# Kernel optimization log

Measured on AMD Instinct MI355X. Metric: run time of the kernel, lower is better.

## Reference

```python
import jax, jax.numpy as jnp
import numpy as np

B, D_IN, D_OUT, E, K, H = 8192, 1024, 1024, 8, 2, 2048


def setup_inputs() -> dict:
    key = jax.random.key(0)
    ks = jax.random.split(key, 7)
    s_in = 1.0 / np.sqrt(D_IN)
    s_h = 1.0 / np.sqrt(H)
    return {
        "x": jax.random.normal(ks[0], (B, D_IN), dtype=jnp.float32),
        "Wg": jax.random.uniform(ks[1], (D_IN, E), minval=-s_in, maxval=s_in, dtype=jnp.float32),
        "bg": jax.random.uniform(ks[2], (E,), minval=-s_in, maxval=s_in, dtype=jnp.float32),
        "W1": jax.random.uniform(ks[3], (E, D_IN, H), minval=-s_in, maxval=s_in, dtype=jnp.float32),
        "b1": jax.random.uniform(ks[4], (E, H), minval=-s_in, maxval=s_in, dtype=jnp.float32),
        "W2": jax.random.uniform(ks[5], (E, H, D_OUT), minval=-s_h, maxval=s_h, dtype=jnp.float32),
        "b2": jax.random.uniform(ks[6], (E, D_OUT), minval=-s_h, maxval=s_h, dtype=jnp.float32),
    }


def reference(x, Wg, bg, W1, b1, W2, b2):
    # gating: linear then top-k -> binary mask (scores are NOT used as weights)
    gate_scores = x @ Wg + bg                      # [B, E]
    _, topk_idx = jax.lax.top_k(gate_scores, K)    # [B, K]
    mask = jax.nn.one_hot(topk_idx, E, dtype=x.dtype).sum(axis=-2)  # [B, E]

    # dense compute of ALL experts (faithful to original module)
    h = jax.nn.relu(jnp.einsum('bi,eih->beh', x, W1) + b1[None])    # [B, E, H]
    expert_out = jnp.einsum('beh,eho->beo', h, W2) + b2[None]       # [B, E, D_OUT]

    # mask to top-k experts and sum over experts
    return jnp.einsum('beo,be->bo', expert_out, mask)               # [B, D_OUT]
```

## Files before the change

### kernel.cpp

```cpp
#include <hip/hip_runtime.h>


#define NTOK 8192
#define DIN  1024
#define DOUT 1024
#define NEXP 8
#define NHID 2048
#define NENT (NTOK * 2)
#define ABLK 64
#define MCHMAX 136

typedef __bf16 bf16_t;
typedef __bf16 bf16x8 __attribute__((ext_vector_type(8)));
typedef __bf16 bf16x4 __attribute__((ext_vector_type(4)));
typedef float  f32x4  __attribute__((ext_vector_type(4)));

#define AS3(p) ((__attribute__((address_space(3))) void*)(unsigned)(unsigned long long)(p))
#define AS1(p) ((__attribute__((address_space(1))) void*)(unsigned long long)(p))

static __device__ __forceinline__ int imin_(int a, int b) { return a < b ? a : b; }

static __device__ __forceinline__ int xcd_swizzle() {
    int cpx = gridDim.x >> 3;
    return (blockIdx.x & 7) * cpx + (blockIdx.x >> 3);
}

__global__ __launch_bounds__(256) void k_transpose_cvt(
    const float* __restrict__ W, bf16_t* __restrict__ WT, int K_, int N_)
{
    __shared__ float tile[64][65];
    const int tilesK = K_ >> 6, tilesN = N_ >> 6;
    int bid = blockIdx.x;
    int e = bid / (tilesK * tilesN);
    int r = bid % (tilesK * tilesN);
    int tk = (r / tilesN) << 6;
    int tn = (r % tilesN) << 6;
    const float* Wb  = W  + (size_t)e * K_ * N_;
    bf16_t*      WTb = WT + (size_t)e * K_ * N_;
    int lr = threadIdx.x >> 6;
    int lc = threadIdx.x & 63;
#pragma unroll
    for (int i = 0; i < 16; ++i) {
        int row = i * 4 + lr;
        tile[row][lc] = Wb[(size_t)(tk + row) * N_ + tn + lc];
    }
    __syncthreads();
#pragma unroll
    for (int i = 0; i < 16; ++i) {
        int row = i * 4 + lr;
        WTb[(size_t)(tn + row) * K_ + tk + lc] = (bf16_t)tile[lc][row];
    }
}

__global__ __launch_bounds__(256) void k_wgT(
    const float* __restrict__ Wg, float* __restrict__ WgT)
{
    int i = blockIdx.x * 256 + threadIdx.x;
    int d = i >> 3, e = i & 7;
    WgT[e * DIN + d] = Wg[i];
}

__global__ __launch_bounds__(256) void k_gating(
    const float* __restrict__ x, const float* __restrict__ WgT,
    const float* __restrict__ bg, bf16_t* __restrict__ xb,
    int* __restrict__ topk)
{
    int lane = threadIdx.x & 63;
    int tok  = blockIdx.x * 4 + (threadIdx.x >> 6);
    const float* xr  = x  + (size_t)tok * DIN;
    bf16_t*      xbr = xb + (size_t)tok * DIN;

    float4 xv[4];
#pragma unroll
    for (int i = 0; i < 4; ++i) {
        int idx = i * 256 + lane * 4;
        xv[i] = *reinterpret_cast<const float4*>(xr + idx);
        bf16x4 o;
        o[0] = (bf16_t)xv[i].x; o[1] = (bf16_t)xv[i].y;
        o[2] = (bf16_t)xv[i].z; o[3] = (bf16_t)xv[i].w;
        *reinterpret_cast<bf16x4*>(xbr + idx) = o;
    }

    float acc[NEXP];
#pragma unroll
    for (int e = 0; e < NEXP; ++e) {
        const float* we = WgT + (size_t)e * DIN;
        float a = 0.f;
#pragma unroll
        for (int i = 0; i < 4; ++i) {
            int idx = i * 256 + lane * 4;
            float4 w = *reinterpret_cast<const float4*>(we + idx);
            a += xv[i].x * w.x + xv[i].y * w.y + xv[i].z * w.z + xv[i].w * w.w;
        }
        acc[e] = a;
    }

#pragma unroll
    for (int e = 0; e < NEXP; ++e) {
#pragma unroll
        for (int off = 32; off >= 1; off >>= 1) acc[e] += __shfl_xor(acc[e], off);
    }
    if (lane == 0) {
        float s[NEXP];
#pragma unroll
        for (int e = 0; e < NEXP; ++e) s[e] = acc[e] + bg[e];
        int e0 = 0;
        for (int e = 1; e < NEXP; ++e) if (s[e] > s[e0]) e0 = e;
        int e1 = (e0 == 0) ? 1 : 0;
        for (int e = 0; e < NEXP; ++e) if (e != e0 && s[e] > s[e1]) e1 = e;
        topk[2 * tok]     = e0;
        topk[2 * tok + 1] = e1;
    }
}

__global__ __launch_bounds__(256) void k_hist(
    const int* __restrict__ topk, int* __restrict__ bh)
{
    __shared__ int h[NEXP];
    if (threadIdx.x < NEXP) h[threadIdx.x] = 0;
    __syncthreads();
    int i = blockIdx.x * 256 + threadIdx.x;
    atomicAdd(&h[topk[i]], 1);
    __syncthreads();
    if (threadIdx.x < NEXP) bh[blockIdx.x * NEXP + threadIdx.x] = h[threadIdx.x];
}

__global__ void k_scan2(const int* __restrict__ bh, int* __restrict__ counts,
                        int* __restrict__ offsets, int* __restrict__ blockbase,
                        int* __restrict__ chtab, int* __restrict__ nch)
{
    __shared__ int sc[NEXP], so_[NEXP + 1];
    int t = threadIdx.x;
    if (t < NEXP) {
        int s = 0;
        for (int b = 0; b < ABLK; ++b) s += bh[b * NEXP + t];
        sc[t] = s;
    }
    __syncthreads();
    if (t == 0) {
        int s = 0;
        for (int e = 0; e < NEXP; ++e) { so_[e] = s; s += sc[e]; }
        so_[NEXP] = s;
        for (int e = 0; e <= NEXP; ++e) offsets[e] = so_[e];
        for (int e = 0; e < NEXP; ++e) counts[e] = sc[e];
    }
    __syncthreads();
    if (t < NEXP) {
        int run = so_[t];
        for (int b = 0; b < ABLK; ++b) {
            blockbase[b * NEXP + t] = run;
            run += bh[b * NEXP + t];
        }
    }
    __syncthreads();
    if (t == 0) {
        int n = 0;
        for (int e = 0; e < NEXP; ++e) {
            int mch = (sc[e] + 127) >> 7;
            for (int m = 0; m < mch; ++m) chtab[n++] = (e << 16) | m;
        }
        nch[0] = n;
    }
}

__global__ __launch_bounds__(256) void k_assign(
    const int* __restrict__ topk, const int* __restrict__ blockbase,
    int* __restrict__ token_ids, int* __restrict__ slot_of)
{
    __shared__ int wcnt[4][NEXP];
    int tid = threadIdx.x, blk = blockIdx.x;
    int i = blk * 256 + tid;
    int e = topk[i];
    int lane = tid & 63, w = tid >> 6;
    unsigned long long ltmask = (1ull << lane) - 1ull;
    int rank_w = 0;
#pragma unroll
    for (int ee = 0; ee < NEXP; ++ee) {
        unsigned long long m = __ballot(e == ee);
        if (ee == e) rank_w = (int)__popcll(m & ltmask);
        if (lane == 0) wcnt[w][ee] = (int)__popcll(m);
    }
    __syncthreads();
    int pre = 0;
    for (int wv = 0; wv < w; ++wv) pre += wcnt[wv][e];
    int s = blockbase[blk * NEXP + e] + pre + rank_w;
    token_ids[s] = i >> 1;
    slot_of[i] = s;
}

__global__ __launch_bounds__(256, 4) void k_gemm1(
    const bf16_t* __restrict__ xb, const bf16_t* __restrict__ w1t,
    const float* __restrict__ b1, bf16_t* __restrict__ hb,
    const int* __restrict__ token_ids, const int* __restrict__ counts,
    const int* __restrict__ offsets, const int* __restrict__ chtab,
    const int* __restrict__ nch)
{
    int bid   = xcd_swizzle();
    int chunk = bid >> 4;
    int nc    = bid & 15;
    if (chunk >= nch[0]) return;
    int em = chtab[chunk];
    int e  = em >> 16;
    int mc = em & 0xffff;
    int count = counts[e];
    int base  = offsets[e];

    __shared__ short At[128][32];
    __shared__ short Bt[128][32];

    int t    = threadIdx.x;
    int lane = t & 63;
    int w    = t >> 6;
    int wr   = (w >> 1) * 64;
    int wc   = (w & 1) * 64;

    int r0 = t >> 2;
    int r1 = 64 + r0;
    int c0 = (t & 3) * 8;

    int row0 = imin_(mc * 128 + r0, count - 1);
    int row1 = imin_(mc * 128 + r1, count - 1);
    const bf16_t* a0 = xb + (size_t)token_ids[base + row0] * DIN + c0;
    const bf16_t* a1 = xb + (size_t)token_ids[base + row1] * DIN + c0;
    const bf16_t* wbase = w1t + (size_t)e * NHID * DIN;
    const bf16_t* bp0 = wbase + (size_t)(nc * 128 + r0) * DIN + c0;
    const bf16_t* bp1 = wbase + (size_t)(nc * 128 + r1) * DIN + c0;

    unsigned lds0 = (unsigned)(t & 192) * 16;
    unsigned lds1 = 4096u + lds0;

    f32x4 acc[4][4];
#pragma unroll
    for (int m = 0; m < 4; ++m)
#pragma unroll
        for (int n = 0; n < 4; ++n) acc[m][n] = (f32x4){0.f, 0.f, 0.f, 0.f};

    char* AtB = (char*)&At[0][0];
    char* BtB = (char*)&Bt[0][0];

    for (int k0 = 0; k0 < DIN; k0 += 32) {
        __builtin_amdgcn_global_load_lds(AS1(a0 + k0),  AS3(AtB + lds0), 16, 0, 0);
        __builtin_amdgcn_global_load_lds(AS1(a1 + k0),  AS3(AtB + lds1), 16, 0, 0);
        __builtin_amdgcn_global_load_lds(AS1(bp0 + k0), AS3(BtB + lds0), 16, 0, 0);
        __builtin_amdgcn_global_load_lds(AS1(bp1 + k0), AS3(BtB + lds1), 16, 0, 0);
        __syncthreads();

        bf16x8 af[4], bfv[4];
        int kr = (lane >> 4) * 8;
#pragma unroll
        for (int m = 0; m < 4; ++m)
            af[m] = *reinterpret_cast<const bf16x8*>(&At[wr + m * 16 + (lane & 15)][kr]);
#pragma unroll
        for (int n = 0; n < 4; ++n)
            bfv[n] = *reinterpret_cast<const bf16x8*>(&Bt[wc + n * 16 + (lane & 15)][kr]);
#pragma unroll
        for (int m = 0; m < 4; ++m)
#pragma unroll
            for (int n = 0; n < 4; ++n)
                acc[m][n] = __builtin_amdgcn_mfma_f32_16x16x32_bf16(af[m], bfv[n], acc[m][n], 0, 0, 0);
        __syncthreads();
    }

    int cl = lane & 15;
    int rq = (lane >> 4) * 4;
#pragma unroll
    for (int n = 0; n < 4; ++n) {
        int col  = nc * 128 + wc + n * 16 + cl;
        float bias = b1[e * NHID + col];
#pragma unroll
        for (int m = 0; m < 4; ++m) {
            int rbase = mc * 128 + wr + m * 16 + rq;
#pragma unroll
            for (int q = 0; q < 4; ++q) {
                int gr = rbase + q;
                if (gr < count) {
                    float v = acc[m][n][q] + bias;
                    v = v > 0.f ? v : 0.f;
                    hb[(size_t)(base + gr) * NHID + col] = (bf16_t)v;
                }
            }
        }
    }
}

__global__ __launch_bounds__(256, 4) void k_gemm2(
    const bf16_t* __restrict__ hb, const bf16_t* __restrict__ w2t,
    bf16_t* __restrict__ so,
    const int* __restrict__ counts, const int* __restrict__ offsets,
    const int* __restrict__ chtab, const int* __restrict__ nch)
{
    int bid   = xcd_swizzle();
    int chunk = bid >> 3;
    int nc    = bid & 7;
    if (chunk >= nch[0]) return;
    int em = chtab[chunk];
    int e  = em >> 16;
    int mc = em & 0xffff;
    int count = counts[e];
    int base  = offsets[e];

    __shared__ short At[128][32];
    __shared__ short Bt[128][32];

    int t    = threadIdx.x;
    int lane = t & 63;
    int w    = t >> 6;
    int wr   = (w >> 1) * 64;
    int wc   = (w & 1) * 64;

    int r0 = t >> 2;
    int r1 = 64 + r0;
    int c0 = (t & 3) * 8;

    int row0 = imin_(mc * 128 + r0, count - 1);
    int row1 = imin_(mc * 128 + r1, count - 1);
    const bf16_t* a0 = hb + (size_t)(base + row0) * NHID + c0;
    const bf16_t* a1 = hb + (size_t)(base + row1) * NHID + c0;
    const bf16_t* wbase = w2t + (size_t)e * DOUT * NHID;
    const bf16_t* bp0 = wbase + (size_t)(nc * 128 + r0) * NHID + c0;
    const bf16_t* bp1 = wbase + (size_t)(nc * 128 + r1) * NHID + c0;

    unsigned lds0 = (unsigned)(t & 192) * 16;
    unsigned lds1 = 4096u + lds0;

    f32x4 acc[4][4];
#pragma unroll
    for (int m = 0; m < 4; ++m)
#pragma unroll
        for (int n = 0; n < 4; ++n) acc[m][n] = (f32x4){0.f, 0.f, 0.f, 0.f};

    char* AtB = (char*)&At[0][0];
    char* BtB = (char*)&Bt[0][0];

    for (int k0 = 0; k0 < NHID; k0 += 32) {
        __builtin_amdgcn_global_load_lds(AS1(a0 + k0),  AS3(AtB + lds0), 16, 0, 0);
        __builtin_amdgcn_global_load_lds(AS1(a1 + k0),  AS3(AtB + lds1), 16, 0, 0);
        __builtin_amdgcn_global_load_lds(AS1(bp0 + k0), AS3(BtB + lds0), 16, 0, 0);
        __builtin_amdgcn_global_load_lds(AS1(bp1 + k0), AS3(BtB + lds1), 16, 0, 0);
        __syncthreads();

        bf16x8 af[4], bfv[4];
        int kr = (lane >> 4) * 8;
#pragma unroll
        for (int m = 0; m < 4; ++m)
            af[m] = *reinterpret_cast<const bf16x8*>(&At[wr + m * 16 + (lane & 15)][kr]);
#pragma unroll
        for (int n = 0; n < 4; ++n)
            bfv[n] = *reinterpret_cast<const bf16x8*>(&Bt[wc + n * 16 + (lane & 15)][kr]);
#pragma unroll
        for (int m = 0; m < 4; ++m)
#pragma unroll
            for (int n = 0; n < 4; ++n)
                acc[m][n] = __builtin_amdgcn_mfma_f32_16x16x32_bf16(af[m], bfv[n], acc[m][n], 0, 0, 0);
        __syncthreads();
    }

    int cl = lane & 15;
    int rq = (lane >> 4) * 4;
#pragma unroll
    for (int n = 0; n < 4; ++n) {
        int col = nc * 128 + wc + n * 16 + cl;
#pragma unroll
        for (int m = 0; m < 4; ++m) {
            int rbase = mc * 128 + wr + m * 16 + rq;
#pragma unroll
            for (int q = 0; q < 4; ++q) {
                int gr = rbase + q;
                if (gr < count)
                    so[(size_t)(base + gr) * DOUT + col] = (bf16_t)acc[m][n][q];
            }
        }
    }
}

__global__ __launch_bounds__(256) void k_combine(
    const bf16_t* __restrict__ so, const float* __restrict__ b2,
    const int* __restrict__ topk, const int* __restrict__ slot_of,
    float* __restrict__ out)
{
    int tid = threadIdx.x;
    int tok = blockIdx.x * 2 + (tid >> 7);
    int c0  = (tid & 127) * 8;
    int s0 = slot_of[2 * tok],  s1 = slot_of[2 * tok + 1];
    int e0 = topk[2 * tok],     e1 = topk[2 * tok + 1];
    bf16x8 a = *reinterpret_cast<const bf16x8*>(so + (size_t)s0 * DOUT + c0);
    bf16x8 b = *reinterpret_cast<const bf16x8*>(so + (size_t)s1 * DOUT + c0);
    const float* bb0 = b2 + (size_t)e0 * DOUT + c0;
    const float* bb1 = b2 + (size_t)e1 * DOUT + c0;
    float* op = out + (size_t)tok * DOUT + c0;
    float4 o0, o1;
    o0.x = (float)a[0] + (float)b[0] + bb0[0] + bb1[0];
    o0.y = (float)a[1] + (float)b[1] + bb0[1] + bb1[1];
    o0.z = (float)a[2] + (float)b[2] + bb0[2] + bb1[2];
    o0.w = (float)a[3] + (float)b[3] + bb0[3] + bb1[3];
    o1.x = (float)a[4] + (float)b[4] + bb0[4] + bb1[4];
    o1.y = (float)a[5] + (float)b[5] + bb0[5] + bb1[5];
    o1.z = (float)a[6] + (float)b[6] + bb0[6] + bb1[6];
    o1.w = (float)a[7] + (float)b[7] + bb0[7] + bb1[7];
    *reinterpret_cast<float4*>(op)     = o0;
    *reinterpret_cast<float4*>(op + 4) = o1;
}

extern "C" void kernel_launch(void* const* d_in, const int* in_sizes, int n_in,
                              void* d_out, int out_size, void* d_ws, size_t ws_size,
                              hipStream_t stream)
{
    const float* x  = (const float*)d_in[0];
    const float* Wg = (const float*)d_in[1];
    const float* bg = (const float*)d_in[2];
    const float* W1 = (const float*)d_in[3];
    const float* b1 = (const float*)d_in[4];
    const float* W2 = (const float*)d_in[5];
    const float* b2 = (const float*)d_in[6];
    float* out = (float*)d_out;

    char* ws = (char*)d_ws;
    bf16_t* xb        = (bf16_t*)(ws);
    bf16_t* w1t       = (bf16_t*)(ws + 16777216);
    bf16_t* w2t       = (bf16_t*)(ws + 50331648);
    bf16_t* hb        = (bf16_t*)(ws + 83886080);
    int*    topk      = (int*)(ws + 150994944);
    int*    counts    = (int*)(ws + 151060480);
    int*    offsets   = (int*)(ws + 151060544);
    int*    token_ids = (int*)(ws + 151060608);
    int*    bh        = (int*)(ws + 151126144);
    int*    blockbase = (int*)(ws + 151128192);
    int*    slot_of   = (int*)(ws + 151130240);

    int* chtab = bh;
    int* nch   = bh + MCHMAX;

    bf16_t* so = (bf16_t*)ws;
    float* wgT = (float*)hb;

    k_wgT<<<(DIN * NEXP) / 256, 256, 0, stream>>>(Wg, wgT);

    k_transpose_cvt<<<NEXP * (DIN / 64) * (NHID / 64), 256, 0, stream>>>(W1, w1t, DIN, NHID);
    k_transpose_cvt<<<NEXP * (NHID / 64) * (DOUT / 64), 256, 0, stream>>>(W2, w2t, NHID, DOUT);

    k_gating<<<NTOK / 4, 256, 0, stream>>>(x, wgT, bg, xb, topk);
    k_hist<<<ABLK, 256, 0, stream>>>(topk, bh);
    k_scan2<<<1, 64, 0, stream>>>(bh, counts, offsets, blockbase, chtab, nch);
    k_assign<<<ABLK, 256, 0, stream>>>(topk, blockbase, token_ids, slot_of);

    k_gemm1<<<MCHMAX * 16, 256, 0, stream>>>(
        xb, w1t, b1, hb, token_ids, counts, offsets, chtab, nch);
    k_gemm2<<<MCHMAX * 8, 256, 0, stream>>>(
        hb, w2t, so, counts, offsets, chtab, nch);
    k_combine<<<NTOK / 2, 256, 0, stream>>>(so, b2, topk, slot_of, out);
}
```

Measured before the change: 312.0 us.

## Triple-buffer LDS tiles in both expert GEMMs with async prefetch pipeline

Both grouped GEMM kernels move from a single LDS tile with load-then-sync-per-iteration to a three-stage ring buffer. Tiles are prefetched two K-steps ahead through global_load_lds, with explicit vmcnt waits and raw s_barrier in place of __syncthreads. The goal is to overlap global memory latency with MFMA work. In exchange LDS use triples to 48KB per block and the launch-bounds occupancy hint drops from 4 to 3 blocks. The hand-written waitcnt and barrier sequence relies on the compiler not reordering or adding vm loads.

Measured after the change: 294.3 us. -5.7%, faster.

```diff
diff --git a/kernel.cpp b/kernel.cpp
--- a/kernel.cpp
+++ b/kernel.cpp
@@ -188,7 +188,7 @@
     slot_of[i] = s;
 }
 
-__global__ __launch_bounds__(256, 4) void k_gemm1(
+__global__ __launch_bounds__(256, 3) void k_gemm1(
     const bf16_t* __restrict__ xb, const bf16_t* __restrict__ w1t,
     const float* __restrict__ b1, bf16_t* __restrict__ hb,
     const int* __restrict__ token_ids, const int* __restrict__ counts,
@@ -205,8 +205,8 @@
     int count = counts[e];
     int base  = offsets[e];
 
-    __shared__ short At[128][32];
-    __shared__ short Bt[128][32];
+    __shared__ short At[3][128][32];
+    __shared__ short Bt[3][128][32];
 
     int t    = threadIdx.x;
     int lane = t & 63;
@@ -235,31 +235,53 @@
 #pragma unroll
         for (int n = 0; n < 4; ++n) acc[m][n] = (f32x4){0.f, 0.f, 0.f, 0.f};
 
-    char* AtB = (char*)&At[0][0];
-    char* BtB = (char*)&Bt[0][0];
-
-    for (int k0 = 0; k0 < DIN; k0 += 32) {
-        __builtin_amdgcn_global_load_lds(AS1(a0 + k0),  AS3(AtB + lds0), 16, 0, 0);
-        __builtin_amdgcn_global_load_lds(AS1(a1 + k0),  AS3(AtB + lds1), 16, 0, 0);
-        __builtin_amdgcn_global_load_lds(AS1(bp0 + k0), AS3(BtB + lds0), 16, 0, 0);
-        __builtin_amdgcn_global_load_lds(AS1(bp1 + k0), AS3(BtB + lds1), 16, 0, 0);
-        __syncthreads();
+    char* AtB = (char*)&At[0][0][0];
+    char* BtB = (char*)&Bt[0][0][0];
+
+#define STAGE1(buf, koff) do {                                                                     \
+    unsigned bo_ = (unsigned)(buf) * 8192u;                                                        \
+    __builtin_amdgcn_global_load_lds(AS1(a0  + (koff)), AS3(AtB + bo_ + lds0), 16, 0, 0);          \
+    __builtin_amdgcn_global_load_lds(AS1(a1  + (koff)), AS3(AtB + bo_ + lds1), 16, 0, 0);          \
+    __builtin_amdgcn_global_load_lds(AS1(bp0 + (koff)), AS3(BtB + bo_ + lds0), 16, 0, 0);          \
+    __builtin_amdgcn_global_load_lds(AS1(bp1 + (koff)), AS3(BtB + bo_ + lds1), 16, 0, 0);          \
+  } while (0)
+
+    constexpr int NK = DIN / 32;
+    STAGE1(0, 0);
+    STAGE1(1, 32);
+    int cc = 0;
+    int cs = 2;
+
+    for (int kt = 0; kt < NK; ++kt) {
+        if (kt + 2 < NK) {
+            STAGE1(cs, (kt + 2) * 32);
+            asm volatile("s_waitcnt vmcnt(8)" ::: "memory");
+        } else if (kt + 2 == NK) {
+            asm volatile("s_waitcnt vmcnt(4)" ::: "memory");
+        } else {
+            asm volatile("s_waitcnt vmcnt(0)" ::: "memory");
+        }
+        __builtin_amdgcn_s_barrier();
 
         bf16x8 af[4], bfv[4];
         int kr = (lane >> 4) * 8;
 #pragma unroll
         for (int m = 0; m < 4; ++m)
-            af[m] = *reinterpret_cast<const bf16x8*>(&At[wr + m * 16 + (lane & 15)][kr]);
+            af[m] = *reinterpret_cast<const bf16x8*>(&At[cc][wr + m * 16 + (lane & 15)][kr]);
 #pragma unroll
         for (int n = 0; n < 4; ++n)
-            bfv[n] = *reinterpret_cast<const bf16x8*>(&Bt[wc + n * 16 + (lane & 15)][kr]);
+            bfv[n] = *reinterpret_cast<const bf16x8*>(&Bt[cc][wc + n * 16 + (lane & 15)][kr]);
 #pragma unroll
         for (int m = 0; m < 4; ++m)
 #pragma unroll
             for (int n = 0; n < 4; ++n)
                 acc[m][n] = __builtin_amdgcn_mfma_f32_16x16x32_bf16(af[m], bfv[n], acc[m][n], 0, 0, 0);
-        __syncthreads();
-    }
+
+        __builtin_amdgcn_s_barrier();
+        cs = cc;
+        cc = (cc == 2) ? 0 : cc + 1;
+    }
+#undef STAGE1
 
     int cl = lane & 15;
     int rq = (lane >> 4) * 4;
@@ -283,7 +305,7 @@
     }
 }
 
-__global__ __launch_bounds__(256, 4) void k_gemm2(
+__global__ __launch_bounds__(256, 3) void k_gemm2(
     const bf16_t* __restrict__ hb, const bf16_t* __restrict__ w2t,
     bf16_t* __restrict__ so,
     const int* __restrict__ counts, const int* __restrict__ offsets,
@@ -299,8 +321,8 @@
     int count = counts[e];
     int base  = offsets[e];
 
-    __shared__ short At[128][32];
-    __shared__ short Bt[128][32];
+    __shared__ short At[3][128][32];
+    __shared__ short Bt[3][128][32];
 
     int t    = threadIdx.x;
     int lane = t & 63;
@@ -329,31 +351,53 @@
 #pragma unroll
         for (int n = 0; n < 4; ++n) acc[m][n] = (f32x4){0.f, 0.f, 0.f, 0.f};
 
-    char* AtB = (char*)&At[0][0];
-    char* BtB = (char*)&Bt[0][0];
-
-    for (int k0 = 0; k0 < NHID; k0 += 32) {
-        __builtin_amdgcn_global_load_lds(AS1(a0 + k0),  AS3(AtB + lds0), 16, 0, 0);
-        __builtin_amdgcn_global_load_lds(AS1(a1 + k0),  AS3(AtB + lds1), 16, 0, 0);
-        __builtin_amdgcn_global_load_lds(AS1(bp0 + k0), AS3(BtB + lds0), 16, 0, 0);
-        __builtin_amdgcn_global_load_lds(AS1(bp1 + k0), AS3(BtB + lds1), 16, 0, 0);
-        __syncthreads();
+    char* AtB = (char*)&At[0][0][0];
+    char* BtB = (char*)&Bt[0][0][0];
+
+#define STAGE2(buf, koff) do {                                                                     \
+    unsigned bo_ = (unsigned)(buf) * 8192u;                                                        \
+    __builtin_amdgcn_global_load_lds(AS1(a0  + (koff)), AS3(AtB + bo_ + lds0), 16, 0, 0);          \
+    __builtin_amdgcn_global_load_lds(AS1(a1  + (koff)), AS3(AtB + bo_ + lds1), 16, 0, 0);          \
+    __builtin_amdgcn_global_load_lds(AS1(bp0 + (koff)), AS3(BtB + bo_ + lds0), 16, 0, 0);          \
+    __builtin_amdgcn_global_load_lds(AS1(bp1 + (koff)), AS3(BtB + bo_ + lds1), 16, 0, 0);          \
+  } while (0)
+
+    constexpr int NK = NHID / 32;
+    STAGE2(0, 0);
+    STAGE2(1, 32);
+    int cc = 0;
+    int cs = 2;
+
+    for (int kt = 0; kt < NK; ++kt) {
+        if (kt + 2 < NK) {
+            STAGE2(cs, (kt + 2) * 32);
+            asm volatile("s_waitcnt vmcnt(8)" ::: "memory");
+        } else if (kt + 2 == NK) {
+            asm volatile("s_waitcnt vmcnt(4)" ::: "memory");
+        } else {
+            asm volatile("s_waitcnt vmcnt(0)" ::: "memory");
+        }
+        __builtin_amdgcn_s_barrier();
 
         bf16x8 af[4], bfv[4];
         int kr = (lane >> 4) * 8;
 #pragma unroll
         for (int m = 0; m < 4; ++m)
-            af[m] = *reinterpret_cast<const bf16x8*>(&At[wr + m * 16 + (lane & 15)][kr]);
+            af[m] = *reinterpret_cast<const bf16x8*>(&At[cc][wr + m * 16 + (lane & 15)][kr]);
 #pragma unroll
         for (int n = 0; n < 4; ++n)
-            bfv[n] = *reinterpret_cast<const bf16x8*>(&Bt[wc + n * 16 + (lane & 15)][kr]);
+            bfv[n] = *reinterpret_cast<const bf16x8*>(&Bt[cc][wc + n * 16 + (lane & 15)][kr]);
 #pragma unroll
         for (int m = 0; m < 4; ++m)
 #pragma unroll
             for (int n = 0; n < 4; ++n)
                 acc[m][n] = __builtin_amdgcn_mfma_f32_16x16x32_bf16(af[m], bfv[n], acc[m][n], 0, 0, 0);
-        __syncthreads();
-    }
+
+        __builtin_amdgcn_s_barrier();
+        cs = cc;
+        cc = (cc == 2) ? 0 : cc + 1;
+    }
+#undef STAGE2
 
     int cl = lane & 15;
     int rq = (lane >> 4) * 4;
```

## Rewrite grouped expert GEMMs with 256x256 tiles, double-buffered LDS and swizzle

Applied to the files above, without the earlier changes.

Both expert GEMMs move from 128x128 tiles with K=32 single-buffered steps to 256x256 tiles with 512 threads, K=64 steps, and double-buffered LDS loaded via global_load_lds. Shared-memory layout uses an XOR swizzle to avoid bank conflicts, and the MFMA phases are interleaved with s_setprio and explicit barriers so the next tile loads while the current one computes. This cuts global/LDS traffic per FLOP and per-iteration sync overhead. The cost is 128KB of LDS per block and fewer blocks, which lowers occupancy and adds padding waste on the last chunk of each expert.

After: 337.2 us. +8.1%, slower.

```diff
diff --git a/kernel.cpp b/kernel.cpp
--- a/kernel.cpp
+++ b/kernel.cpp
@@ -8,7 +8,7 @@
 #define NHID 2048
 #define NENT (NTOK * 2)
 #define ABLK 64
-#define MCHMAX 136
+#define MCHMAX 72
 
 typedef __bf16 bf16_t;
 typedef __bf16 bf16x8 __attribute__((ext_vector_type(8)));
@@ -156,7 +156,7 @@
     if (t == 0) {
         int n = 0;
         for (int e = 0; e < NEXP; ++e) {
-            int mch = (sc[e] + 127) >> 7;
+            int mch = (sc[e] + 255) >> 8;
             for (int m = 0; m < mch; ++m) chtab[n++] = (e << 16) | m;
         }
         nch[0] = n;
@@ -188,106 +188,64 @@
     slot_of[i] = s;
 }
 
-__global__ __launch_bounds__(256, 4) void k_gemm1(
+
+#define GEMM_PHASES(NKV)                                                           \
+    for (int kt = 0; kt < NKV; ++kt) {                                             \
+        const short* Ac = &As[kt & 1][0][0];                                       \
+        const short* Bc = &Bs[kt & 1][0][0];                                       \
+        unsigned dstb = (unsigned)(((kt & 1) ^ 1) * 32768) + wb;                   \
+        bf16x8 b_[4][2];                                                           \
+        _Pragma("unroll")                                                          \
+        for (int ph = 0; ph < 4; ++ph) {                                           \
+            if (ph == 0) {                                                         \
+                if (kt + 1 < NKV) {                                                \
+                    int ko = (kt + 1) * 64;                                        \
+                    __builtin_amdgcn_global_load_lds(AS1(aP0 + ko), AS3(AB + dstb),         16, 0, 0); \
+                    __builtin_amdgcn_global_load_lds(AS1(aP1 + ko), AS3(AB + dstb + 8192),  16, 0, 0); \
+                    __builtin_amdgcn_global_load_lds(AS1(aP2 + ko), AS3(AB + dstb + 16384), 16, 0, 0); \
+                    __builtin_amdgcn_global_load_lds(AS1(aP3 + ko), AS3(AB + dstb + 24576), 16, 0, 0); \
+                    __builtin_amdgcn_global_load_lds(AS1(bP0 + ko), AS3(BB + dstb),         16, 0, 0); \
+                    __builtin_amdgcn_global_load_lds(AS1(bP1 + ko), AS3(BB + dstb + 8192),  16, 0, 0); \
+                    __builtin_amdgcn_global_load_lds(AS1(bP2 + ko), AS3(BB + dstb + 16384), 16, 0, 0); \
+                    __builtin_amdgcn_global_load_lds(AS1(bP3 + ko), AS3(BB + dstb + 24576), 16, 0, 0); \
+                }                                                                  \
+                _Pragma("unroll")                                                  \
+                for (int nf = 0; nf < 4; ++nf) {                                   \
+                    b_[nf][0] = *reinterpret_cast<const bf16x8*>(Bc + nf * 1024 + boff0);        \
+                    b_[nf][1] = *reinterpret_cast<const bf16x8*>(Bc + nf * 1024 + (boff0 ^ 32)); \
+                }                                                                  \
+            }                                                                      \
+            bf16x8 a_[2][2];                                                       \
+            _Pragma("unroll")                                                      \
+            for (int j = 0; j < 2; ++j) {                                          \
+                const short* ar = Ac + (ph * 2 + j) * 1024;                        \
+                a_[j][0] = *reinterpret_cast<const bf16x8*>(ar + aoff0);           \
+                a_[j][1] = *reinterpret_cast<const bf16x8*>(ar + (aoff0 ^ 32));    \
+            }                                                                      \
+            __builtin_amdgcn_s_barrier();                                          \
+            __builtin_amdgcn_s_setprio(1);                                         \
+            _Pragma("unroll")                                                      \
+            for (int j = 0; j < 2; ++j) {                                          \
+                _Pragma("unroll")                                                  \
+                for (int nf = 0; nf < 4; ++nf) {                                   \
+                    acc[ph * 2 + j][nf] = __builtin_amdgcn_mfma_f32_16x16x32_bf16( \
+                        a_[j][0], b_[nf][0], acc[ph * 2 + j][nf], 0, 0, 0);        \
+                    acc[ph * 2 + j][nf] = __builtin_amdgcn_mfma_f32_16x16x32_bf16( \
+                        a_[j][1], b_[nf][1], acc[ph * 2 + j][nf], 0, 0, 0);        \
+                }                                                                  \
+            }                                                                      \
+            __builtin_amdgcn_s_setprio(0);                                         \
+            if (ph == 3) asm volatile("s_waitcnt vmcnt(0)" ::: "memory");          \
+            __builtin_amdgcn_s_barrier();                                          \
+        }                                                                          \
+    }
+
+__global__ __launch_bounds__(512) void k_gemm1(
     const bf16_t* __restrict__ xb, const bf16_t* __restrict__ w1t,
     const float* __restrict__ b1, bf16_t* __restrict__ hb,
     const int* __restrict__ token_ids, const int* __restrict__ counts,
     const int* __restrict__ offsets, const int* __restrict__ chtab,
     const int* __restrict__ nch)
-{
-    int bid   = xcd_swizzle();
-    int chunk = bid >> 4;
-    int nc    = bid & 15;
-    if (chunk >= nch[0]) return;
-    int em = chtab[chunk];
-    int e  = em >> 16;
-    int mc = em & 0xffff;
-    int count = counts[e];
-    int base  = offsets[e];
-
-    __shared__ short At[128][32];
-    __shared__ short Bt[128][32];
-
-    int t    = threadIdx.x;
-    int lane = t & 63;
-    int w    = t >> 6;
-    int wr   = (w >> 1) * 64;
-    int wc   = (w & 1) * 64;
-
-    int r0 = t >> 2;
-    int r1 = 64 + r0;
-    int c0 = (t & 3) * 8;
-
-    int row0 = imin_(mc * 128 + r0, count - 1);
-    int row1 = imin_(mc * 128 + r1, count - 1);
-    const bf16_t* a0 = xb + (size_t)token_ids[base + row0] * DIN + c0;
-    const bf16_t* a1 = xb + (size_t)token_ids[base + row1] * DIN + c0;
-    const bf16_t* wbase = w1t + (size_t)e * NHID * DIN;
-    const bf16_t* bp0 = wbase + (size_t)(nc * 128 + r0) * DIN + c0;
-    const bf16_t* bp1 = wbase + (size_t)(nc * 128 + r1) * DIN + c0;
-
-    unsigned lds0 = (unsigned)(t & 192) * 16;
-    unsigned lds1 = 4096u + lds0;
-
-    f32x4 acc[4][4];
-#pragma unroll
-    for (int m = 0; m < 4; ++m)
-#pragma unroll
-        for (int n = 0; n < 4; ++n) acc[m][n] = (f32x4){0.f, 0.f, 0.f, 0.f};
-
-    char* AtB = (char*)&At[0][0];
-    char* BtB = (char*)&Bt[0][0];
-
-    for (int k0 = 0; k0 < DIN; k0 += 32) {
-        __builtin_amdgcn_global_load_lds(AS1(a0 + k0),  AS3(AtB + lds0), 16, 0, 0);
-        __builtin_amdgcn_global_load_lds(AS1(a1 + k0),  AS3(AtB + lds1), 16, 0, 0);
-        __builtin_amdgcn_global_load_lds(AS1(bp0 + k0), AS3(BtB + lds0), 16, 0, 0);
-        __builtin_amdgcn_global_load_lds(AS1(bp1 + k0), AS3(BtB + lds1), 16, 0, 0);
-        __syncthreads();
-
-        bf16x8 af[4], bfv[4];
-        int kr = (lane >> 4) * 8;
-#pragma unroll
-        for (int m = 0; m < 4; ++m)
-            af[m] = *reinterpret_cast<const bf16x8*>(&At[wr + m * 16 + (lane & 15)][kr]);
-#pragma unroll
-        for (int n = 0; n < 4; ++n)
-            bfv[n] = *reinterpret_cast<const bf16x8*>(&Bt[wc + n * 16 + (lane & 15)][kr]);
-#pragma unroll
-        for (int m = 0; m < 4; ++m)
-#pragma unroll
-            for (int n = 0; n < 4; ++n)
-                acc[m][n] = __builtin_amdgcn_mfma_f32_16x16x32_bf16(af[m], bfv[n], acc[m][n], 0, 0, 0);
-        __syncthreads();
-    }
-
-    int cl = lane & 15;
-    int rq = (lane >> 4) * 4;
-#pragma unroll
-    for (int n = 0; n < 4; ++n) {
-        int col  = nc * 128 + wc + n * 16 + cl;
-        float bias = b1[e * NHID + col];
-#pragma unroll
-        for (int m = 0; m < 4; ++m) {
-            int rbase = mc * 128 + wr + m * 16 + rq;
-#pragma unroll
-            for (int q = 0; q < 4; ++q) {
-                int gr = rbase + q;
-                if (gr < count) {
-                    float v = acc[m][n][q] + bias;
-                    v = v > 0.f ? v : 0.f;
-                    hb[(size_t)(base + gr) * NHID + col] = (bf16_t)v;
-                }
-            }
-        }
-    }
-}
-
-__global__ __launch_bounds__(256, 4) void k_gemm2(
-    const bf16_t* __restrict__ hb, const bf16_t* __restrict__ w2t,
-    bf16_t* __restrict__ so,
-    const int* __restrict__ counts, const int* __restrict__ offsets,
-    const int* __restrict__ chtab, const int* __restrict__ nch)
 {
     int bid   = xcd_swizzle();
     int chunk = bid >> 3;
@@ -299,75 +257,167 @@
     int count = counts[e];
     int base  = offsets[e];
 
-    __shared__ short At[128][32];
-    __shared__ short Bt[128][32];
+    __shared__ short As[2][256][64];
+    __shared__ short Bs[2][256][64];
 
     int t    = threadIdx.x;
+    int w    = t >> 6;
     int lane = t & 63;
+    int wrM  = (w >> 2) * 128;
+    int wcN  = (w & 3) * 64;
+    int lm   = lane & 15;
+    int kq   = lane >> 4;
+    int ru   = lane & 7;
+
+    int aoff0 = (wrM + lm) * 64 + ((kq ^ ru) * 8);
+    int boff0 = (wcN + lm) * 64 + ((kq ^ ru) * 8);
+
+    int rbase = t >> 3;
+    int c0s   = ((t & 7) ^ ((t >> 3) & 7)) * 8;
+    unsigned wb = (unsigned)(w * 1024);
+
+    const bf16_t* wgt = w1t + (size_t)e * NHID * DIN;
+    int r0 = imin_(mc * 256 +   0 + rbase, count - 1);
+    int r1 = imin_(mc * 256 +  64 + rbase, count - 1);
+    int r2 = imin_(mc * 256 + 128 + rbase, count - 1);
+    int r3 = imin_(mc * 256 + 192 + rbase, count - 1);
+    const bf16_t* aP0 = xb + (size_t)token_ids[base + r0] * DIN + c0s;
+    const bf16_t* aP1 = xb + (size_t)token_ids[base + r1] * DIN + c0s;
+    const bf16_t* aP2 = xb + (size_t)token_ids[base + r2] * DIN + c0s;
+    const bf16_t* aP3 = xb + (size_t)token_ids[base + r3] * DIN + c0s;
+    const bf16_t* bP0 = wgt + (size_t)(nc * 256 +   0 + rbase) * DIN + c0s;
+    const bf16_t* bP1 = wgt + (size_t)(nc * 256 +  64 + rbase) * DIN + c0s;
+    const bf16_t* bP2 = wgt + (size_t)(nc * 256 + 128 + rbase) * DIN + c0s;
+    const bf16_t* bP3 = wgt + (size_t)(nc * 256 + 192 + rbase) * DIN + c0s;
+
+    char* AB = (char*)&As[0][0][0];
+    char* BB = (char*)&Bs[0][0][0];
+
+    f32x4 acc[8][4];
+#pragma unroll
+    for (int m = 0; m < 8; ++m)
+#pragma unroll
+        for (int n = 0; n < 4; ++n) acc[m][n] = (f32x4){0.f, 0.f, 0.f, 0.f};
+
+    __builtin_amdgcn_global_load_lds(AS1(aP0), AS3(AB + wb),         16, 0, 0);
+    __builtin_amdgcn_global_load_lds(AS1(aP1), AS3(AB + wb + 8192),  16, 0, 0);
+    __builtin_amdgcn_global_load_lds(AS1(aP2), AS3(AB + wb + 16384), 16, 0, 0);
+    __builtin_amdgcn_global_load_lds(AS1(aP3), AS3(AB + wb + 24576), 16, 0, 0);
+    __builtin_amdgcn_global_load_lds(AS1(bP0), AS3(BB + wb),         16, 0, 0);
+    __builtin_amdgcn_global_load_lds(AS1(bP1), AS3(BB + wb + 8192),  16, 0, 0);
+    __builtin_amdgcn_global_load_lds(AS1(bP2), AS3(BB + wb + 16384), 16, 0, 0);
+    __builtin_amdgcn_global_load_lds(AS1(bP3), AS3(BB + wb + 24576), 16, 0, 0);
+    asm volatile("s_waitcnt vmcnt(0)" ::: "memory");
+    __builtin_amdgcn_s_barrier();
+
+    constexpr int NK = DIN / 64;
+    GEMM_PHASES(NK)
+
+    int rq = kq * 4;
+#pragma unroll
+    for (int nf = 0; nf < 4; ++nf) {
+        int col  = nc * 256 + wcN + nf * 16 + lm;
+        float bias = b1[e * NHID + col];
+#pragma unroll
+        for (int mf = 0; mf < 8; ++mf) {
+            int gr0 = mc * 256 + wrM + mf * 16 + rq;
+#pragma unroll
+            for (int q = 0; q < 4; ++q) {
+                int gr = gr0 + q;
+                if (gr < count) {
+                    float v = acc[mf][nf][q] + bias;
+                    v = v > 0.f ? v : 0.f;
+                    hb[(size_t)(base + gr) * NHID + col] = (bf16_t)v;
+                }
+            }
+        }
+    }
+}
+
+__global__ __launch_bounds__(512) void k_gemm2(
+    const bf16_t* __restrict__ hb, const bf16_t* __restrict__ w2t,
+    bf16_t* __restrict__ so,
+    const int* __restrict__ counts, const int* __restrict__ offsets,
+    const int* __restrict__ chtab, const int* __restrict__ nch)
+{
+    int bid   = xcd_swizzle();
+    int chunk = bid >> 2;
+    int nc    = bid & 3;
+    if (chunk >= nch[0]) return;
+    int em = chtab[chunk];
+    int e  = em >> 16;
+    int mc = em & 0xffff;
+    int count = counts[e];
+    int base  = offsets[e];
+
+    __shared__ short As[2][256][64];
+    __shared__ short Bs[2][256][64];
+
+    int t    = threadIdx.x;
     int w    = t >> 6;
-    int wr   = (w >> 1) * 64;
-    int wc   = (w & 1) * 64;
-
-    int r0 = t >> 2;
-    int r1 = 64 + r0;
-    int c0 = (t & 3) * 8;
-
-    int row0 = imin_(mc * 128 + r0, count - 1);
-    int row1 = imin_(mc * 128 + r1, count - 1);
-    const bf16_t* a0 = hb + (size_t)(base + row0) * NHID + c0;
-    const bf16_t* a1 = hb + (size_t)(base + row1) * NHID + c0;
-    const bf16_t* wbase = w2t + (size_t)e * DOUT * NHID;
-    const bf16_t* bp0 = wbase + (size_t)(nc * 128 + r0) * NHID + c0;
-    const bf16_t* bp1 = wbase + (size_t)(nc * 128 + r1) * NHID + c0;
-
-    unsigned lds0 = (unsigned)(t & 192) * 16;
-    unsigned lds1 = 4096u + lds0;
-
-    f32x4 acc[4][4];
-#pragma unroll
-    for (int m = 0; m < 4; ++m)
+    int lane = t & 63;
+    int wrM  = (w >> 2) * 128;
+    int wcN  = (w & 3) * 64;
+    int lm   = lane & 15;
+    int kq   = lane >> 4;
+    int ru   = lane & 7;
+
+    int aoff0 = (wrM + lm) * 64 + ((kq ^ ru) * 8);
+    int boff0 = (wcN + lm) * 64 + ((kq ^ ru) * 8);
+
+    int rbase = t >> 3;
+    int c0s   = ((t & 7) ^ ((t >> 3) & 7)) * 8;
+    unsigned wb = (unsigned)(w * 1024);
+
+    const bf16_t* wgt = w2t + (size_t)e * DOUT * NHID;
+    int r0 = imin_(mc * 256 +   0 + rbase, count - 1);
+    int r1 = imin_(mc * 256 +  64 + rbase, count - 1);
+    int r2 = imin_(mc * 256 + 128 + rbase, count - 1);
+    int r3 = imin_(mc * 256 + 192 + rbase, count - 1);
+    const bf16_t* aP0 = hb + (size_t)(base + r0) * NHID + c0s;
+    const bf16_t* aP1 = hb + (size_t)(base + r1) * NHID + c0s;
+    const bf16_t* aP2 = hb + (size_t)(base + r2) * NHID + c0s;
+    const bf16_t* aP3 = hb + (size_t)(base + r3) * NHID + c0s;
+    const bf16_t* bP0 = wgt + (size_t)(nc * 256 +   0 + rbase) * NHID + c0s;
+    const bf16_t* bP1 = wgt + (size_t)(nc * 256 +  64 + rbase) * NHID + c0s;
+    const bf16_t* bP2 = wgt + (size_t)(nc * 256 + 128 + rbase) * NHID + c0s;
+    const bf16_t* bP3 = wgt + (size_t)(nc * 256 + 192 + rbase) * NHID + c0s;
+
+    char* AB = (char*)&As[0][0][0];
+    char* BB = (char*)&Bs[0][0][0];
+
+    f32x4 acc[8][4];
+#pragma unroll
+    for (int m = 0; m < 8; ++m)
 #pragma unroll
         for (int n = 0; n < 4; ++n) acc[m][n] = (f32x4){0.f, 0.f, 0.f, 0.f};
 
-    char* AtB = (char*)&At[0][0];
-    char* BtB = (char*)&Bt[0][0];
-
-    for (int k0 = 0; k0 < NHID; k0 += 32) {
-        __builtin_amdgcn_global_load_lds(AS1(a0 + k0),  AS3(AtB + lds0), 16, 0, 0);
-        __builtin_amdgcn_global_load_lds(AS1(a1 + k0),  AS3(AtB + lds1), 16, 0, 0);
-        __builtin_amdgcn_global_load_lds(AS1(bp0 + k0), AS3(BtB + lds0), 16, 0, 0);
-        __builtin_amdgcn_global_load_lds(AS1(bp1 + k0), AS3(BtB + lds1), 16, 0, 0);
-        __syncthreads();
-
-        bf16x8 af[4], bfv[4];
-        int kr = (lane >> 4) * 8;
-#pragma unroll
-        for (int m = 0; m < 4; ++m)
-            af[m] = *reinterpret_cast<const bf16x8*>(&At[wr + m * 16 + (lane & 15)][kr]);
-#pragma unroll
-        for (int n = 0; n < 4; ++n)
-            bfv[n] = *reinterpret_cast<const bf16x8*>(&Bt[wc + n * 16 + (lane & 15)][kr]);
-#pragma unroll
-        for (int m = 0; m < 4; ++m)
-#pragma unroll
-            for (int n = 0; n < 4; ++n)
-                acc[m][n] = __builtin_amdgcn_mfma_f32_16x16x32_bf16(af[m], bfv[n], acc[m][n], 0, 0, 0);
-        __syncthreads();
-    }
-
-    int cl = lane & 15;
-    int rq = (lane >> 4) * 4;
-#pragma unroll
-    for (int n = 0; n < 4; ++n) {
-        int col = nc * 128 + wc + n * 16 + cl;
-#pragma unroll
-        for (int m = 0; m < 4; ++m) {
-            int rbase = mc * 128 + wr + m * 16 + rq;
+    __builtin_amdgcn_global_load_lds(AS1(aP0), AS3(AB + wb),         16, 0, 0);
+    __builtin_amdgcn_global_load_lds(AS1(aP1), AS3(AB + wb + 8192),  16, 0, 0);
+    __builtin_amdgcn_global_load_lds(AS1(aP2), AS3(AB + wb + 16384), 16, 0, 0);
+    __builtin_amdgcn_global_load_lds(AS1(aP3), AS3(AB + wb + 24576), 16, 0, 0);
+    __builtin_amdgcn_global_load_lds(AS1(bP0), AS3(BB + wb),         16, 0, 0);
+    __builtin_amdgcn_global_load_lds(AS1(bP1), AS3(BB + wb + 8192),  16, 0, 0);
+    __builtin_amdgcn_global_load_lds(AS1(bP2), AS3(BB + wb + 16384), 16, 0, 0);
+    __builtin_amdgcn_global_load_lds(AS1(bP3), AS3(BB + wb + 24576), 16, 0, 0);
+    asm volatile("s_waitcnt vmcnt(0)" ::: "memory");
+    __builtin_amdgcn_s_barrier();
+
+    constexpr int NK = NHID / 64;
+    GEMM_PHASES(NK)
+
+    int rq = kq * 4;
+#pragma unroll
+    for (int nf = 0; nf < 4; ++nf) {
+        int col = nc * 256 + wcN + nf * 16 + lm;
+#pragma unroll
+        for (int mf = 0; mf < 8; ++mf) {
+            int gr0 = mc * 256 + wrM + mf * 16 + rq;
 #pragma unroll
             for (int q = 0; q < 4; ++q) {
-                int gr = rbase + q;
+                int gr = gr0 + q;
                 if (gr < count)
-                    so[(size_t)(base + gr) * DOUT + col] = (bf16_t)acc[m][n][q];
+                    so[(size_t)(base + gr) * DOUT + col] = (bf16_t)acc[mf][nf][q];
             }
         }
     }
@@ -443,9 +493,9 @@
     k_scan2<<<1, 64, 0, stream>>>(bh, counts, offsets, blockbase, chtab, nch);
     k_assign<<<ABLK, 256, 0, stream>>>(topk, blockbase, token_ids, slot_of);
 
-    k_gemm1<<<MCHMAX * 16, 256, 0, stream>>>(
+    k_gemm1<<<MCHMAX * 8, 512, 0, stream>>>(
         xb, w1t, b1, hb, token_ids, counts, offsets, chtab, nch);
-    k_gemm2<<<MCHMAX * 8, 256, 0, stream>>>(
+    k_gemm2<<<MCHMAX * 4, 512, 0, stream>>>(
         hb, w2t, so, counts, offsets, chtab, nch);
     k_combine<<<NTOK / 2, 256, 0, stream>>>(so, b2, topk, slot_of, out);
 }
```
